# Kernel tuning notes

Measured on AMD Instinct MI355X. Metric: run time of the kernel, lower is better.

Reference implementation:

```python
import jax, jax.numpy as jnp
import numpy as np

N_EXPERT = 64
EMBD_DIM = 4096
TOP_K = 8
NEG_INF = -1e30  # stand-in for -inf, safe in fp16/bf16 softmax


def setup_inputs() -> dict:
    key = jax.random.key(0)
    kx, kw = jax.random.split(key)
    x = jax.random.normal(kx, (4, 4096, EMBD_DIM), dtype=jnp.float32)
    # nn.Linear weight: [out_features, in_features] = [n_expert, embd_dim]
    W = jax.random.normal(kw, (N_EXPERT, EMBD_DIM), dtype=jnp.float32) / np.sqrt(EMBD_DIM)
    return {"x": x, "W": W}


def reference(x, W):
    # logits = x @ W^T : [b, s, e]
    logits = jnp.einsum('bsd,ed->bse', x, W)
    top_k_logits, indices = jax.lax.top_k(logits, TOP_K)  # [b,s,k]
    # scatter top-k logits into a -inf tensor == keep logits where selected, -inf elsewhere
    mask = jnp.any(indices[..., None] == jnp.arange(N_EXPERT), axis=-2)  # [b,s,e] bool
    masked = jnp.where(mask, logits, NEG_INF)
    probs = jax.nn.softmax(masked, axis=-1)
    return probs, indices
```

## Files before the change

### kernel.cpp

```cpp
#include <hip/hip_runtime.h>
#include <math.h>

#define TOKENS 16384
#define EMBD   4096
#define NEXP   64
#define TOPK   8
#define KSPLIT 8
#define KSLICE (EMBD / KSPLIT)
#define CHUNK  16
#define EHALF  32

__global__ void transpose_w(const float* __restrict__ W, float* __restrict__ Wt) {
    int idx = blockIdx.x * blockDim.x + threadIdx.x;
    int e = idx >> 12;
    int k = idx & 4095;
    Wt[k * NEXP + e] = W[idx];
}

__global__ __launch_bounds__(256, 3) void gemm_partial(
    const float* __restrict__ x, const float* __restrict__ Wt,
    float* __restrict__ part) {
    const int lane = threadIdx.x & 63;
    const int wave = threadIdx.x >> 6;
    const int tgrp = wave >> 1;
    const int half = __builtin_amdgcn_readfirstlane(wave & 1);
    const int tok  = blockIdx.x * 128 + tgrp * 64 + lane;
    const int ks   = blockIdx.y;
    const int kbase = ks * KSLICE;

    const float* xrow  = x + (size_t)tok * EMBD + kbase;
    const float* wbase = Wt + (size_t)kbase * NEXP + half * EHALF;

    double accd[EHALF];
#pragma unroll
    for (int e = 0; e < EHALF; ++e) accd[e] = 0.0;

    for (int kc = 0; kc < KSLICE; kc += CHUNK) {
        const float4* xp = (const float4*)(xrow + kc);
        float4 a = xp[0], b = xp[1], c = xp[2], d4 = xp[3];
        float xv[CHUNK] = {a.x, a.y, a.z, a.w,  b.x, b.y, b.z, b.w,
                           c.x, c.y, c.z, c.w,  d4.x, d4.y, d4.z, d4.w};

        float accf[EHALF];
#pragma unroll
        for (int e = 0; e < EHALF; ++e) accf[e] = 0.0f;

#pragma unroll
        for (int j = 0; j < CHUNK; ++j) {
            const float xj = xv[j];
            const float* wrow = wbase + (size_t)(kc + j) * NEXP;
#pragma unroll
            for (int e = 0; e < EHALF; ++e)
                accf[e] = fmaf(wrow[e], xj, accf[e]);
        }

#pragma unroll
        for (int e = 0; e < EHALF; ++e) accd[e] += (double)accf[e];
    }

    float4* dst = (float4*)(part + ((size_t)ks * TOKENS + tok) * NEXP
                            + (size_t)half * EHALF);
#pragma unroll
    for (int v = 0; v < EHALF / 4; ++v)
        dst[v] = make_float4((float)accd[4 * v],     (float)accd[4 * v + 1],
                             (float)accd[4 * v + 2], (float)accd[4 * v + 3]);
}

__global__ __launch_bounds__(256) void topk_softmax(
    const float* __restrict__ part, float* __restrict__ probs,
    float* __restrict__ idxout) {
    __shared__ float lval[4][NEXP];
    __shared__ float lidx[4][TOPK];

    const int lane = threadIdx.x & 63;
    const int wave = threadIdx.x >> 6;
    const int tok  = blockIdx.x * 4 + wave;

    double d = 0.0;
#pragma unroll
    for (int s = 0; s < KSPLIT; ++s)
        d += (double)part[((size_t)s * TOKENS + tok) * NEXP + lane];
    const float logit = (float)d;

    lval[wave][lane] = logit;
    __syncthreads();

    const float4* lv4 = (const float4*)lval[wave];
    int rank = 0;
    float m = -INFINITY;
#pragma unroll
    for (int q4 = 0; q4 < NEXP / 4; ++q4) {
        float4 v = lv4[q4];
        const int qb = q4 * 4;
        rank += (v.x > logit || (v.x == logit && qb + 0 < lane)) ? 1 : 0;
        rank += (v.y > logit || (v.y == logit && qb + 1 < lane)) ? 1 : 0;
        rank += (v.z > logit || (v.z == logit && qb + 2 < lane)) ? 1 : 0;
        rank += (v.w > logit || (v.w == logit && qb + 3 < lane)) ? 1 : 0;
        m = fmaxf(fmaxf(m, v.x), fmaxf(v.y, fmaxf(v.z, v.w)));
    }

    const bool sel = rank < TOPK;
    const float t  = sel ? expf(logit - m) : 0.0f;

    float denom = t;
#pragma unroll
    for (int off = 32; off > 0; off >>= 1)
        denom += __shfl_xor(denom, off);

    if (sel) lidx[wave][rank] = (float)lane;
    __syncthreads();

    probs[(size_t)tok * NEXP + lane] = sel ? (t / denom) : 0.0f;
    if (lane < TOPK) idxout[(size_t)tok * TOPK + lane] = lidx[wave][lane];
}

extern "C" void kernel_launch(void* const* d_in, const int* in_sizes, int n_in,
                              void* d_out, int out_size, void* d_ws, size_t ws_size,
                              hipStream_t stream) {
    const float* x = (const float*)d_in[0];
    const float* W = (const float*)d_in[1];

    float* out    = (float*)d_out;
    float* probs  = out;
    float* idxout = out + (size_t)TOKENS * NEXP;

    float* Wt   = (float*)d_ws;
    float* part = Wt + (size_t)EMBD * NEXP;

    hipLaunchKernelGGL(transpose_w, dim3((EMBD * NEXP) / 256), dim3(256), 0, stream,
                       W, Wt);
    hipLaunchKernelGGL(gemm_partial, dim3(TOKENS / 128, KSPLIT), dim3(256), 0, stream,
                       x, Wt, part);
    hipLaunchKernelGGL(topk_softmax, dim3(TOKENS / 4), dim3(256), 0, stream,
                       part, probs, idxout);
}
```

Baseline: 436.2 us.

## Split experts into quarters per wave and prefetch next x chunk

Each block now handles 64 tokens with four waves, each wave computing 16 experts instead of 32. That halves accumulator registers and allows higher occupancy (launch bounds raised to 4). The x row chunk for the next iteration is software-prefetched into registers before the current FMAs run. The trade-off is that each token's x row is now read by four waves instead of two, which doubles the x traffic through the cache hierarchy on an input of roughly 256 MB.

```diff
diff --git a/kernel.cpp b/kernel.cpp
--- a/kernel.cpp
+++ b/kernel.cpp
@@ -8,7 +8,7 @@
 #define KSPLIT 8
 #define KSLICE (EMBD / KSPLIT)
 #define CHUNK  16
-#define EHALF  32
+#define EQTR   16
 
 __global__ void transpose_w(const float* __restrict__ W, float* __restrict__ Wt) {
     int idx = blockIdx.x * blockDim.x + threadIdx.x;
@@ -17,51 +17,60 @@
     Wt[k * NEXP + e] = W[idx];
 }
 
-__global__ __launch_bounds__(256, 3) void gemm_partial(
+__global__ __launch_bounds__(256, 4) void gemm_partial(
     const float* __restrict__ x, const float* __restrict__ Wt,
     float* __restrict__ part) {
     const int lane = threadIdx.x & 63;
     const int wave = threadIdx.x >> 6;
-    const int tgrp = wave >> 1;
-    const int half = __builtin_amdgcn_readfirstlane(wave & 1);
-    const int tok  = blockIdx.x * 128 + tgrp * 64 + lane;
+    const int qtr  = __builtin_amdgcn_readfirstlane(wave);
+    const int tok  = blockIdx.x * 64 + lane;
     const int ks   = blockIdx.y;
     const int kbase = ks * KSLICE;
 
     const float* xrow  = x + (size_t)tok * EMBD + kbase;
-    const float* wbase = Wt + (size_t)kbase * NEXP + half * EHALF;
+    const float* wbase = Wt + (size_t)kbase * NEXP + qtr * EQTR;
 
-    double accd[EHALF];
+    double accd[EQTR];
 #pragma unroll
-    for (int e = 0; e < EHALF; ++e) accd[e] = 0.0;
+    for (int e = 0; e < EQTR; ++e) accd[e] = 0.0;
 
+    float4 n0, n1, n2, n3;
+    {
+        const float4* xp = (const float4*)xrow;
+        n0 = xp[0]; n1 = xp[1]; n2 = xp[2]; n3 = xp[3];
+    }
+
+#pragma unroll 2
     for (int kc = 0; kc < KSLICE; kc += CHUNK) {
-        const float4* xp = (const float4*)(xrow + kc);
-        float4 a = xp[0], b = xp[1], c = xp[2], d4 = xp[3];
+        float4 a = n0, b = n1, c = n2, d4 = n3;
+        const int kcn = (kc + CHUNK < KSLICE) ? kc + CHUNK : 0;
+        const float4* xp = (const float4*)(xrow + kcn);
+        n0 = xp[0]; n1 = xp[1]; n2 = xp[2]; n3 = xp[3];
+
         float xv[CHUNK] = {a.x, a.y, a.z, a.w,  b.x, b.y, b.z, b.w,
                            c.x, c.y, c.z, c.w,  d4.x, d4.y, d4.z, d4.w};
 
-        float accf[EHALF];
+        float accf[EQTR];
 #pragma unroll
-        for (int e = 0; e < EHALF; ++e) accf[e] = 0.0f;
+        for (int e = 0; e < EQTR; ++e) accf[e] = 0.0f;
 
 #pragma unroll
         for (int j = 0; j < CHUNK; ++j) {
             const float xj = xv[j];
             const float* wrow = wbase + (size_t)(kc + j) * NEXP;
 #pragma unroll
-            for (int e = 0; e < EHALF; ++e)
+            for (int e = 0; e < EQTR; ++e)
                 accf[e] = fmaf(wrow[e], xj, accf[e]);
         }
 
 #pragma unroll
-        for (int e = 0; e < EHALF; ++e) accd[e] += (double)accf[e];
+        for (int e = 0; e < EQTR; ++e) accd[e] += (double)accf[e];
     }
 
     float4* dst = (float4*)(part + ((size_t)ks * TOKENS + tok) * NEXP
-                            + (size_t)half * EHALF);
+                            + (size_t)qtr * EQTR);
 #pragma unroll
-    for (int v = 0; v < EHALF / 4; ++v)
+    for (int v = 0; v < EQTR / 4; ++v)
         dst[v] = make_float4((float)accd[4 * v],     (float)accd[4 * v + 1],
                              (float)accd[4 * v + 2], (float)accd[4 * v + 3]);
 }
@@ -129,7 +138,7 @@
 
     hipLaunchKernelGGL(transpose_w, dim3((EMBD * NEXP) / 256), dim3(256), 0, stream,
                        W, Wt);
-    hipLaunchKernelGGL(gemm_partial, dim3(TOKENS / 128, KSPLIT), dim3(256), 0, stream,
+    hipLaunchKernelGGL(gemm_partial, dim3(TOKENS / 64, KSPLIT), dim3(256), 0, stream,
                        x, Wt, part);
     hipLaunchKernelGGL(topk_softmax, dim3(TOKENS / 4), dim3(256), 0, stream,
                        part, probs, idxout);
```

Result: slower. 473.9 us (+8.6%).
